# Optimization experiments

Measured on AMD Instinct MI355X. Metric: run time of the kernel, lower is better.

The kernel has to match this reference:

```python
import jax, jax.numpy as jnp
import numpy as np

N, E, B, H = 20000, 100000, 512, 64
IN_CH, EDGE_DIM, OUT_CH = 16, 8, 1


def setup_inputs() -> dict:
    key = jax.random.key(0)
    ks = jax.random.split(key, 20)
    rn = lambda k, shp, s=0.1: (jax.random.normal(k, shp, jnp.float32) * s)
    return {
        'x': rn(ks[0], (N, IN_CH), 1.0),
        'edge_index': jax.random.randint(ks[1], (2, E), 0, N),
        'edge_attr': rn(ks[2], (E, EDGE_DIM), 1.0),
        'batch': jnp.sort(jax.random.randint(ks[3], (N,), 0, B)),
        'lin0_w': rn(ks[4], (IN_CH, H)), 'lin0_b': jnp.zeros((H,), jnp.float32),
        'nn1_w': rn(ks[5], (EDGE_DIM, 128)), 'nn1_b': jnp.zeros((128,), jnp.float32),
        'nn2_w': rn(ks[6], (128, H * H), 0.02), 'nn2_b': jnp.zeros((H * H,), jnp.float32),
        'root_w': rn(ks[7], (H, H)), 'root_b': jnp.zeros((H,), jnp.float32),
        'gru_wih': rn(ks[8], (H, 3 * H)), 'gru_whh': rn(ks[9], (H, 3 * H)),
        'gru_bih': jnp.zeros((3 * H,), jnp.float32), 'gru_bhh': jnp.zeros((3 * H,), jnp.float32),
        'lstm_wih': rn(ks[10], (2 * H, 4 * H)), 'lstm_whh': rn(ks[11], (H, 4 * H)),
        'lstm_bih': jnp.zeros((4 * H,), jnp.float32), 'lstm_bhh': jnp.zeros((4 * H,), jnp.float32),
        'lin1_w': rn(ks[12], (2 * H, H)), 'lin1_b': jnp.zeros((H,), jnp.float32),
        'lin2_w': rn(ks[13], (H, OUT_CH)), 'lin2_b': jnp.zeros((OUT_CH,), jnp.float32),
    }


def reference(x, edge_index, edge_attr, batch, lin0_w, lin0_b, nn1_w, nn1_b,
              nn2_w, nn2_b, root_w, root_b, gru_wih, gru_whh, gru_bih, gru_bhh,
              lstm_wih, lstm_whh, lstm_bih, lstm_bhh, lin1_w, lin1_b, lin2_w, lin2_b):
    src, dst = edge_index[0], edge_index[1]
    # edge network weights (shared across the 3 message-passing steps)
    ew = jax.nn.relu(edge_attr @ nn1_w + nn1_b) @ nn2_w + nn2_b  # [E, H*H]
    ew = ew.reshape(E, H, H)
    deg = jnp.maximum(jax.ops.segment_sum(jnp.ones((E,), x.dtype), dst, N), 1.0)

    out = jax.nn.relu(x @ lin0_w + lin0_b)  # [N, H]
    h = out
    for _ in range(3):
        # NNConv: gather src feats, per-edge matvec, scatter-mean to dst, + root linear
        msg = jnp.einsum('ei,eio->eo', out[src], ew)                  # [E, H]
        agg = jax.ops.segment_sum(msg, dst, N) / deg[:, None]          # [N, H]
        m = jax.nn.relu(agg + out @ root_w + root_b)
        # GRU cell (torch gate order r, z, n)
        gi = m @ gru_wih + gru_bih
        gh = h @ gru_whh + gru_bhh
        r = jax.nn.sigmoid(gi[:, :H] + gh[:, :H])
        z = jax.nn.sigmoid(gi[:, H:2 * H] + gh[:, H:2 * H])
        n = jnp.tanh(gi[:, 2 * H:] + r * gh[:, 2 * H:])
        h = (1.0 - z) * n + z * h
        out = h

    # Set2Set pooling, 3 processing steps (torch LSTM gate order i, f, g, o)
    q_star = jnp.zeros((B, 2 * H), x.dtype)
    hh = jnp.zeros((B, H), x.dtype)
    cc = jnp.zeros((B, H), x.dtype)
    for _ in range(3):
        g = q_star @ lstm_wih + hh @ lstm_whh + lstm_bih + lstm_bhh    # [B, 4H]
        i_g = jax.nn.sigmoid(g[:, :H])
        f_g = jax.nn.sigmoid(g[:, H:2 * H])
        g_g = jnp.tanh(g[:, 2 * H:3 * H])
        o_g = jax.nn.sigmoid(g[:, 3 * H:])
        cc = f_g * cc + i_g * g_g
        hh = o_g * jnp.tanh(cc)
        q = hh                                                          # [B, H]
        e = jnp.sum(out * q[batch], axis=-1)                            # [N]
        e_max = jax.ops.segment_max(e, batch, B)
        a = jnp.exp(e - e_max[batch])
        a = a / jax.ops.segment_sum(a, batch, B)[batch]
        rvec = jax.ops.segment_sum(a[:, None] * out, batch, B)          # [B, H]
        q_star = jnp.concatenate([q, rvec], axis=-1)

    y = jax.nn.relu(q_star @ lin1_w + lin1_b) @ lin2_w + lin2_b         # [B, 1]
    return y
```

## Files before the change

kernel.cpp:

```cpp
#include <hip/hip_runtime.h>
#include <hip/hip_bf16.h>
#include <hip/hip_fp16.h>
#include <cstddef>
#include <cstdint>

#define N_NODES 20000
#define N_EDGES 100000
#define N_BATCH 512

#define EPB 96
#define TS 6
#define ECAP 100032

typedef __attribute__((ext_vector_type(8))) short ushort8_t;
typedef __attribute__((ext_vector_type(8))) _Float16 f16x8;
typedef __attribute__((ext_vector_type(4))) float f32x4;

union F16x8U { f16x8 v; unsigned int u[4]; };

__device__ __forceinline__ float sigmoidf_(float x) { return 1.f / (1.f + expf(-x)); }
__device__ __forceinline__ unsigned short f2h(float x) {
    return __half_as_ushort(__float2half(x));
}
__device__ __forceinline__ float h2f(unsigned short s) {
    return __half2float(__ushort_as_half(s));
}

#define LIN0_BLOCKS 5000
#define BSW_BLOCKS 258
#define CNT_BLOCKS 391

__global__ __launch_bounds__(256) void prep1_kernel(
        const float* __restrict__ x, const float* __restrict__ l0w, const float* __restrict__ l0b,
        const float* __restrict__ w2, const float* __restrict__ b2,
        const int* __restrict__ ei,
        float* __restrict__ out, unsigned short* __restrict__ bsw,
        int* __restrict__ cnt, int E) {
    int bid = blockIdx.x, tid = threadIdx.x;
    if (bid < LIN0_BLOCKS) {
        int idx = bid * 256 + tid;
        int n = idx >> 6, j = idx & 63;
        float acc = l0b[j];
#pragma unroll
        for (int i = 0; i < 16; i++) acc += x[n * 16 + i] * l0w[i * 64 + j];
        out[idx] = fmaxf(acc, 0.f);
    } else if (bid < LIN0_BLOCKS + BSW_BLOCKS) {
        int idx = (bid - LIN0_BLOCKS) * 256 + tid;
        if (idx < 66048) {
            int l = idx & 63, oc = (idx >> 6) & 3, ks = idx >> 8;
            int o = oc * 16 + (l & 15);
            int kap0 = ks * 32 + 8 * (l >> 4);
#pragma unroll
            for (int j = 0; j < 8; ++j) {
                int kap = kap0 + j;
                int k = kap >> 6, i = kap & 63;
                float v = (k < 128) ? w2[(size_t)k * 4096 + i * 64 + o] : b2[i * 64 + o];
                bsw[(size_t)idx * 8 + j] = f2h(v);
            }
        }
    } else {
        int e = (bid - LIN0_BLOCKS - BSW_BLOCKS) * 256 + tid;
        if (e < E) atomicAdd(&cnt[ei[E + e]], 1);
    }
}

__global__ __launch_bounds__(1024) void scan_kernel(const int* __restrict__ cnt,
                                                    int* __restrict__ cstart,
                                                    int* __restrict__ cursor,
                                                    float* __restrict__ degf, int n) {
    __shared__ int part[1024];
    int t = threadIdx.x;
    int base = t * 20;
    int loc[20];
    int s = 0;
#pragma unroll
    for (int i = 0; i < 20; ++i) {
        int idx = base + i;
        int c = (idx < n) ? cnt[idx] : 0;
        loc[i] = s;
        s += c;
    }
    part[t] = s;
    __syncthreads();
    for (int off = 1; off < 1024; off <<= 1) {
        int v = (t >= off) ? part[t - off] : 0;
        __syncthreads();
        part[t] += v;
        __syncthreads();
    }
    int tb = part[t] - s;
#pragma unroll
    for (int i = 0; i < 20; ++i) {
        int idx = base + i;
        if (idx < n) {
            int b0 = tb + loc[i];
            cstart[idx] = b0;
            cursor[idx] = b0;
            degf[idx] = (float)cnt[idx];
        }
    }
}

__global__ void place_kernel(const int* __restrict__ ei, const float* __restrict__ ea,
                             int* __restrict__ cursor,
                             int* __restrict__ src_s, float* __restrict__ ea_s, int E) {
    int e = blockIdx.x * 256 + threadIdx.x;
    if (e < E) {
        int dst = ei[E + e];
        int slot = atomicAdd(&cursor[dst], 1);
        src_s[slot] = ei[e];
        const float4* s = (const float4*)(ea + (size_t)e * 8);
        float4 a = s[0], b = s[1];
        float4* d = (float4*)(ea_s + (size_t)slot * 8);
        d[0] = a; d[1] = b;
    }
}

__global__ __launch_bounds__(256, 2) void msg_mfma(const float* __restrict__ out,
                                                   const float* __restrict__ ea_s,
                                                   const float* __restrict__ w1g,
                                                   const float* __restrict__ b1g,
                                                   const unsigned short* __restrict__ bsw,
                                                   const int* __restrict__ src_s,
                                                   unsigned short* __restrict__ msgp, int E) {
    __shared__ __align__(16) unsigned short hs16[128 * EPB];
    __shared__ __align__(16) float w1l[8 * 128];
    __shared__ __align__(16) float b1l[128];
    const int tid = threadIdx.x;
    const int w = tid >> 6, l = tid & 63;
    const int e0 = blockIdx.x * EPB;
    const int r16 = l & 15, q = l >> 4;

    {
        f32x4 v = *(const f32x4*)&w1g[tid * 4];
        *(f32x4*)&w1l[tid * 4] = v;
        if (tid < 32) *(f32x4*)&b1l[tid * 4] = *(const f32x4*)&b1g[tid * 4];
    }

    f16x8 sfrag[TS][2];
#pragma unroll
    for (int t = 0; t < TS; ++t) {
        int e = e0 + t * 16 + r16;
        int src = (e < E) ? src_s[e] : 0;
        const f32x4* p = (const f32x4*)(out + (size_t)src * 64);
#pragma unroll
        for (int st = 0; st < 2; ++st) {
            f16x8 f = {};
            if (e < E) {
                f32x4 a = p[st * 8 + q * 2], b = p[st * 8 + q * 2 + 1];
#pragma unroll
                for (int j = 0; j < 4; ++j) { f[j] = (_Float16)a[j]; f[4 + j] = (_Float16)b[j]; }
            }
            sfrag[t][st] = f;
        }
    }

    __syncthreads();

    if (tid < 192) {
        int ep = tid >> 1;
        int koff = (tid & 1) * 64;
        int e = e0 + ep;
        bool v = e < E;
        float ear[8];
        const float* earow = ea_s + (size_t)(v ? e : 0) * 8;
#pragma unroll
        for (int i = 0; i < 8; ++i) ear[i] = earow[i];
#pragma unroll
        for (int kv = 0; kv < 16; ++kv) {
            int k = koff + kv * 4;
            f32x4 a = *(const f32x4*)&b1l[k];
#pragma unroll
            for (int i = 0; i < 8; ++i) {
                f32x4 wv = *(const f32x4*)&w1l[i * 128 + k];
                a += ear[i] * wv;
            }
#pragma unroll
            for (int jj = 0; jj < 4; ++jj)
                hs16[(k + jj) * EPB + ep] = v ? f2h(fmaxf(a[jj], 0.f)) : (unsigned short)0;
        }
    }

    const f16x8* bp = (const f16x8*)bsw;
    f16x8 bfA[8], bfB[8];
#pragma unroll
    for (int i = 0; i < 8; ++i) bfA[i] = bp[((w * 8 + i) << 6) + l];

    __syncthreads();

    f32x4 acc[TS][4] = {};

#define MSG_COMPUTE(K, BF)                                                     \
    {                                                                          \
        _Pragma("unroll")                                                      \
        for (int t = 0; t < TS; ++t) {                                         \
            unsigned int hu = hs16[(K) * EPB + t * 16 + r16];                  \
            _Pragma("unroll")                                                  \
            for (int st = 0; st < 2; ++st) {                                   \
                F16x8U s_, a_;                                                 \
                s_.v = sfrag[t][st];                                           \
                asm("v_pk_mul_f16 %0, %1, %2 op_sel:[0,0] op_sel_hi:[0,1]"     \
                    : "=v"(a_.u[0]) : "v"(hu), "v"(s_.u[0]));                  \
                asm("v_pk_mul_f16 %0, %1, %2 op_sel:[0,0] op_sel_hi:[0,1]"     \
                    : "=v"(a_.u[1]) : "v"(hu), "v"(s_.u[1]));                  \
                asm("v_pk_mul_f16 %0, %1, %2 op_sel:[0,0] op_sel_hi:[0,1]"     \
                    : "=v"(a_.u[2]) : "v"(hu), "v"(s_.u[2]));                  \
                asm("v_pk_mul_f16 %0, %1, %2 op_sel:[0,0] op_sel_hi:[0,1]"     \
                    : "=v"(a_.u[3]) : "v"(hu), "v"(s_.u[3]));                  \
                _Pragma("unroll")                                              \
                for (int oc = 0; oc < 4; ++oc)                                 \
                    acc[t][oc] = __builtin_amdgcn_mfma_f32_16x16x32_f16(       \
                        a_.v, BF[st * 4 + oc], acc[t][oc], 0, 0, 0);           \
            }                                                                  \
        }                                                                      \
    }

#pragma unroll 1
    for (int kk = 0; kk < 16; ++kk) {
        int k1 = w + kk * 8;
        int k2 = k1 + 4;
#pragma unroll
        for (int i = 0; i < 8; ++i) bfB[i] = bp[((k2 * 8 + i) << 6) + l];
        MSG_COMPUTE(k1, bfA);
        if (kk < 15) {
            int k3 = k1 + 8;
#pragma unroll
            for (int i = 0; i < 8; ++i) bfA[i] = bp[((k3 * 8 + i) << 6) + l];
        }
        MSG_COMPUTE(k2, bfB);
    }
#undef MSG_COMPUTE

    if (w == 0) {
#pragma unroll
        for (int i = 0; i < 8; ++i) bfA[i] = bp[((128 * 8 + i) << 6) + l];
#pragma unroll
        for (int t = 0; t < TS; ++t)
#pragma unroll
            for (int st = 0; st < 2; ++st)
#pragma unroll
                for (int oc = 0; oc < 4; ++oc)
                    acc[t][oc] = __builtin_amdgcn_mfma_f32_16x16x32_f16(
                        sfrag[t][st], bfA[st * 4 + oc], acc[t][oc], 0, 0, 0);
    }

    unsigned short* slab = msgp + (size_t)w * ECAP * 64;
#pragma unroll
    for (int t = 0; t < TS; ++t) {
#pragma unroll
        for (int r = 0; r < 4; ++r) {
            int e = e0 + t * 16 + q * 4 + r;
            if (e < E) {
                unsigned short* row = slab + (size_t)e * 64 + r16;
                row[0]  = f2h(acc[t][0][r]);
                row[16] = f2h(acc[t][1][r]);
                row[32] = f2h(acc[t][2][r]);
                row[48] = f2h(acc[t][3][r]);
            }
        }
    }
}

__global__ __launch_bounds__(256) void gru_kernel(float* __restrict__ out,
                                                  const unsigned short* __restrict__ msgp,
                                                  const int* __restrict__ cstart,
                                                  const int* __restrict__ cnt,
                                                  const float* __restrict__ deg,
                                                  const float* __restrict__ root_w,
                                                  const float* __restrict__ root_b,
                                                  const float* __restrict__ wih,
                                                  const float* __restrict__ whh,
                                                  const float* __restrict__ bih,
                                                  const float* __restrict__ bhh) {
    int w = threadIdx.x >> 6, j = threadIdx.x & 63;
    int n = blockIdx.x * 4 + w;
    __shared__ float s_o[4][64];
    __shared__ float s_m[4][64];
    s_o[w][j] = out[(size_t)n * 64 + j];
    __syncthreads();

    float msum = 0.f;
    {
        int base = cstart[n], c = cnt[n];
        for (int s2 = 0; s2 < c; ++s2) {
            size_t slot = (size_t)(base + s2) * 64 + j;
            float a0 = h2f(msgp[slot]);
            float a1 = h2f(msgp[(size_t)ECAP * 64 + slot]);
            float a2 = h2f(msgp[2 * (size_t)ECAP * 64 + slot]);
            float a3 = h2f(msgp[3 * (size_t)ECAP * 64 + slot]);
            msum += (a0 + a1) + (a2 + a3);
        }
    }
    float d = deg[n]; if (d < 1.f) d = 1.f;
    float mv = msum / d + root_b[j];
#pragma unroll 8
    for (int i = 0; i < 64; i++) mv += s_o[w][i] * root_w[i * 64 + j];
    mv = fmaxf(mv, 0.f);
    s_m[w][j] = mv;
    __syncthreads();
    float gi_r = bih[j], gi_z = bih[64 + j], gi_n = bih[128 + j];
    float gh_r = bhh[j], gh_z = bhh[64 + j], gh_n = bhh[128 + j];
#pragma unroll 4
    for (int i = 0; i < 64; i++) {
        float m = s_m[w][i], hv = s_o[w][i];
        gi_r += m * wih[i * 192 + j];
        gi_z += m * wih[i * 192 + 64 + j];
        gi_n += m * wih[i * 192 + 128 + j];
        gh_r += hv * whh[i * 192 + j];
        gh_z += hv * whh[i * 192 + 64 + j];
        gh_n += hv * whh[i * 192 + 128 + j];
    }
    float r = sigmoidf_(gi_r + gh_r);
    float z = sigmoidf_(gi_z + gh_z);
    float nn = tanhf(gi_n + r * gh_n);
    float hnew = (1.f - z) * nn + z * s_o[w][j];
    out[(size_t)n * 64 + j] = hnew;
}

__global__ __launch_bounds__(256) void s2s_final(const float* __restrict__ out,
                                                 const int* __restrict__ batch,
                                                 const float* __restrict__ wih,
                                                 const float* __restrict__ whh,
                                                 const float* __restrict__ bih,
                                                 const float* __restrict__ bhh,
                                                 const float* __restrict__ w1,
                                                 const float* __restrict__ b1,
                                                 const float* __restrict__ w2,
                                                 const float* __restrict__ b2,
                                                 float* __restrict__ y, int N) {
    int b = blockIdx.x;
    int tid = threadIdx.x;
    int gate = tid >> 6, j = tid & 63;
    __shared__ float s_qs[128];
    __shared__ float s_g[4][64];
    __shared__ float s_h[64];
    __shared__ float s_c[64];
    __shared__ int s_lo, s_hi;
    __shared__ float s_red[4];
    __shared__ float s_rv[4][64];

    if (tid < 128) s_qs[tid] = 0.f;
    if (gate == 2) s_h[j] = 0.f;
    if (gate == 3) s_c[j] = 0.f;
    if (tid == 0) {
        int lo = 0, hi = N;
        while (lo < hi) { int mid = (lo + hi) >> 1; if (batch[mid] < b) lo = mid + 1; else hi = mid; }
        s_lo = lo;
        int lo2 = lo, hi2 = N;
        while (lo2 < hi2) { int mid = (lo2 + hi2) >> 1; if (batch[mid] < b + 1) lo2 = mid + 1; else hi2 = mid; }
        s_hi = lo2;
    }
    __syncthreads();

    for (int it = 0; it < 3; ++it) {
        float g = bih[gate * 64 + j] + bhh[gate * 64 + j];
#pragma unroll 4
        for (int i = 0; i < 128; ++i) g += s_qs[i] * wih[i * 256 + gate * 64 + j];
#pragma unroll 4
        for (int i = 0; i < 64; ++i) g += s_h[i] * whh[i * 256 + gate * 64 + j];
        s_g[gate][j] = g;
        __syncthreads();
        if (gate == 0) {
            float c = sigmoidf_(s_g[1][j]) * s_c[j] + sigmoidf_(s_g[0][j]) * tanhf(s_g[2][j]);
            float h = sigmoidf_(s_g[3][j]) * tanhf(c);
            s_c[j] = c;
            s_h[j] = h;
            s_qs[j] = h;
        }
        __syncthreads();

        int lo = s_lo, hi = s_hi;
        float wmax = -3.402823e38f;
        for (int n = lo + gate; n < hi; n += 4) {
            float p = out[(size_t)n * 64 + j] * s_h[j];
#pragma unroll
            for (int d = 32; d >= 1; d >>= 1) p += __shfl_xor(p, d);
            wmax = fmaxf(wmax, p);
        }
        if (j == 0) s_red[gate] = wmax;
        __syncthreads();
        float m = fmaxf(fmaxf(s_red[0], s_red[1]), fmaxf(s_red[2], s_red[3]));
        __syncthreads();
        float ssum = 0.f, rv = 0.f;
        for (int n = lo + gate; n < hi; n += 4) {
            float xv = out[(size_t)n * 64 + j];
            float p = xv * s_h[j];
#pragma unroll
            for (int d = 32; d >= 1; d >>= 1) p += __shfl_xor(p, d);
            float a = expf(p - m);
            ssum += a;
            rv += a * xv;
        }
        if (j == 0) s_red[gate] = ssum;
        s_rv[gate][j] = rv;
        __syncthreads();
        if (gate == 0) {
            float S = s_red[0] + s_red[1] + s_red[2] + s_red[3];
            float r = s_rv[0][j] + s_rv[1][j] + s_rv[2][j] + s_rv[3][j];
            s_qs[64 + j] = (S > 0.f) ? r / S : 0.f;
        }
        __syncthreads();
    }

    if (gate == 0) {
        float tv = b1[j];
#pragma unroll 4
        for (int i = 0; i < 128; ++i) tv += s_qs[i] * w1[i * 64 + j];
        tv = fmaxf(tv, 0.f);
        float p = tv * w2[j];
#pragma unroll
        for (int d = 32; d >= 1; d >>= 1) p += __shfl_xor(p, d);
        if (j == 0) y[b] = p + b2[0];
    }
}

extern "C" void kernel_launch(void* const* d_in, const int* in_sizes, int n_in,
                              void* d_out, int out_size, void* d_ws, size_t ws_size,
                              hipStream_t stream) {
    const int N = N_NODES, E = N_EDGES, B = N_BATCH;
    const float* x       = (const float*)d_in[0];
    const int*   ei      = (const int*)d_in[1];
    const float* ea      = (const float*)d_in[2];
    const int*   batch   = (const int*)d_in[3];
    const float* lin0_w  = (const float*)d_in[4];
    const float* lin0_b  = (const float*)d_in[5];
    const float* nn1_w   = (const float*)d_in[6];
    const float* nn1_b   = (const float*)d_in[7];
    const float* nn2_w   = (const float*)d_in[8];
    const float* nn2_b   = (const float*)d_in[9];
    const float* root_w  = (const float*)d_in[10];
    const float* root_b  = (const float*)d_in[11];
    const float* gru_wih = (const float*)d_in[12];
    const float* gru_whh = (const float*)d_in[13];
    const float* gru_bih = (const float*)d_in[14];
    const float* gru_bhh = (const float*)d_in[15];
    const float* lstm_wih = (const float*)d_in[16];
    const float* lstm_whh = (const float*)d_in[17];
    const float* lstm_bih = (const float*)d_in[18];
    const float* lstm_bhh = (const float*)d_in[19];
    const float* lin1_w  = (const float*)d_in[20];
    const float* lin1_b  = (const float*)d_in[21];
    const float* lin2_w  = (const float*)d_in[22];
    const float* lin2_b  = (const float*)d_in[23];
    float* y = (float*)d_out;

    char* ws = (char*)d_ws;
    size_t off = 0;
    auto alloc = [&](size_t bytes) { void* p = ws + off; off = (off + bytes + 255) & ~(size_t)255; return p; };
    unsigned short* bsw  = (unsigned short*)alloc((size_t)66048 * 8 * 2);
    unsigned short* msgp = (unsigned short*)alloc((size_t)4 * ECAP * 64 * 2);
    float* ea_s   = (float*)alloc((size_t)ECAP * 8 * 4);
    float* out    = (float*)alloc((size_t)N * 64 * 4);
    float* deg    = (float*)alloc((size_t)N * 4);
    int*   cnt    = (int*)alloc((size_t)N * 4);
    int*   cstart = (int*)alloc((size_t)N * 4);
    int*   cursor = (int*)alloc((size_t)N * 4);
    int*   src_s  = (int*)alloc((size_t)E * 4);

    hipMemsetAsync(cnt, 0, (size_t)N * 4, stream);

    prep1_kernel<<<LIN0_BLOCKS + BSW_BLOCKS + CNT_BLOCKS, 256, 0, stream>>>(
        x, lin0_w, lin0_b, nn2_w, nn2_b, ei, out, bsw, cnt, E);
    scan_kernel<<<1, 1024, 0, stream>>>(cnt, cstart, cursor, deg, N);
    place_kernel<<<(E + 255) / 256, 256, 0, stream>>>(ei, ea, cursor, src_s, ea_s, E);

    for (int step = 0; step < 3; ++step) {
        msg_mfma<<<(E + EPB - 1) / EPB, 256, 0, stream>>>(out, ea_s, nn1_w, nn1_b,
                                                          bsw, src_s, msgp, E);
        gru_kernel<<<N / 4, 256, 0, stream>>>(out, msgp, cstart, cnt, deg, root_w, root_b,
                                              gru_wih, gru_whh, gru_bih, gru_bhh);
    }

    s2s_final<<<B, 256, 0, stream>>>(out, batch, lstm_wih, lstm_whh, lstm_bih, lstm_bhh,
                                     lin1_w, lin1_b, lin2_w, lin2_b, y, N);
}
```

Measured before the change: 671.7 us.

## Split msg_mfma by edges across waves with LDS double-buffered weight staging

Before, each wave handled a slice of the hidden dimension k for all 96 edges in the block, and wrote a partial-sum slab that the GRU kernel had to add up across four slabs. Now each wave owns 32 of the 128 edges in the block and loops over all 129 k values. The nn2 weight fragments are staged into LDS with global_load_lds, double-buffered and separated by barriers. The root/bias term is folded in by adding a constant-one row to hs16, and a single message buffer removes the four-slab write and read traffic. The cost is a block barrier on every k iteration and fewer MFMA tiles per wave, with occupancy raised to 3 blocks per multiprocessor to hide the latency.

```diff
diff --git a/kernel.cpp b/kernel.cpp
--- a/kernel.cpp
+++ b/kernel.cpp
@@ -8,9 +8,8 @@
 #define N_EDGES 100000
 #define N_BATCH 512
 
-#define EPB 96
-#define TS 6
-#define ECAP 100032
+#define EPB 128
+#define ECAP 100096
 
 typedef __attribute__((ext_vector_type(8))) short ushort8_t;
 typedef __attribute__((ext_vector_type(8))) _Float16 f16x8;
@@ -116,20 +115,23 @@
     }
 }
 
-__global__ __launch_bounds__(256, 2) void msg_mfma(const float* __restrict__ out,
+__global__ __launch_bounds__(256, 3) void msg_mfma(const float* __restrict__ out,
                                                    const float* __restrict__ ea_s,
                                                    const float* __restrict__ w1g,
                                                    const float* __restrict__ b1g,
                                                    const unsigned short* __restrict__ bsw,
                                                    const int* __restrict__ src_s,
                                                    unsigned short* __restrict__ msgp, int E) {
-    __shared__ __align__(16) unsigned short hs16[128 * EPB];
-    __shared__ __align__(16) float w1l[8 * 128];
-    __shared__ __align__(16) float b1l[128];
+    __shared__ __align__(16) unsigned short hs16[129 * EPB];
+    __shared__ __align__(16) unsigned char bbuf[2 * 8192];
+    float* w1l = (float*)bbuf;
+    float* b1l = (float*)(bbuf + 4096);
+
     const int tid = threadIdx.x;
     const int w = tid >> 6, l = tid & 63;
     const int e0 = blockIdx.x * EPB;
     const int r16 = l & 15, q = l >> 4;
+    const int w32 = w * 32;
 
     {
         f32x4 v = *(const f32x4*)&w1g[tid * 4];
@@ -137,10 +139,10 @@
         if (tid < 32) *(f32x4*)&b1l[tid * 4] = *(const f32x4*)&b1g[tid * 4];
     }
 
-    f16x8 sfrag[TS][2];
-#pragma unroll
-    for (int t = 0; t < TS; ++t) {
-        int e = e0 + t * 16 + r16;
+    f16x8 sfrag[2][2];
+#pragma unroll
+    for (int t = 0; t < 2; ++t) {
+        int e = e0 + w32 + t * 16 + r16;
         int src = (e < E) ? src_s[e] : 0;
         const f32x4* p = (const f32x4*)(out + (size_t)src * 64);
 #pragma unroll
@@ -157,9 +159,9 @@
 
     __syncthreads();
 
-    if (tid < 192) {
-        int ep = tid >> 1;
-        int koff = (tid & 1) * 64;
+    {
+        int ep = tid & 127;
+        int koff = (tid >> 7) * 64;
         int e = e0 + ep;
         bool v = e < E;
         float ear[8];
@@ -179,22 +181,36 @@
             for (int jj = 0; jj < 4; ++jj)
                 hs16[(k + jj) * EPB + ep] = v ? f2h(fmaxf(a[jj], 0.f)) : (unsigned short)0;
         }
-    }
-
-    const f16x8* bp = (const f16x8*)bsw;
-    f16x8 bfA[8], bfB[8];
-#pragma unroll
-    for (int i = 0; i < 8; ++i) bfA[i] = bp[((w * 8 + i) << 6) + l];
-
-    __syncthreads();
-
-    f32x4 acc[TS][4] = {};
-
-#define MSG_COMPUTE(K, BF)                                                     \
+        if (koff == 0)
+            hs16[128 * EPB + ep] = v ? (unsigned short)0x3C00 : (unsigned short)0;
+    }
+
+    __syncthreads();
+
+    typedef __attribute__((address_space(3))) void lds_t;
+    typedef const __attribute__((address_space(1))) void gm_t;
+
+#define STAGE(SLOT, BUF)                                                       \
     {                                                                          \
         _Pragma("unroll")                                                      \
-        for (int t = 0; t < TS; ++t) {                                         \
-            unsigned int hu = hs16[(K) * EPB + t * 16 + r16];                  \
+        for (int i = 0; i < 2; ++i) {                                          \
+            int fr = 2 * w + i;                                                \
+            const unsigned short* g = bsw + (((size_t)(SLOT) * 8 + fr) * 64 + l) * 8; \
+            __builtin_amdgcn_global_load_lds((gm_t*)g,                         \
+                (lds_t*)(bbuf + (BUF) * 8192 + fr * 1024), 16, 0, 0);          \
+        }                                                                      \
+    }
+
+#define COMPUTE(K, BUF)                                                        \
+    {                                                                          \
+        const f16x8* bP = (const f16x8*)(bbuf + (BUF) * 8192);                 \
+        f16x8 bf[8];                                                           \
+        _Pragma("unroll")                                                      \
+        for (int i = 0; i < 8; ++i) bf[i] = bP[i * 64 + l];                    \
+        __builtin_amdgcn_s_setprio(1);                                         \
+        _Pragma("unroll")                                                      \
+        for (int t = 0; t < 2; ++t) {                                          \
+            unsigned int hu = hs16[(K) * EPB + w32 + t * 16 + r16];            \
             _Pragma("unroll")                                                  \
             for (int st = 0; st < 2; ++st) {                                   \
                 F16x8U s_, a_;                                                 \
@@ -210,48 +226,40 @@
                 _Pragma("unroll")                                              \
                 for (int oc = 0; oc < 4; ++oc)                                 \
                     acc[t][oc] = __builtin_amdgcn_mfma_f32_16x16x32_f16(       \
-                        a_.v, BF[st * 4 + oc], acc[t][oc], 0, 0, 0);           \
+                        a_.v, bf[st * 4 + oc], acc[t][oc], 0, 0, 0);           \
             }                                                                  \
         }                                                                      \
-    }
+        __builtin_amdgcn_s_setprio(0);                                         \
+    }
+
+    STAGE(0, 0);
+
+    f32x4 acc[2][4] = {};
 
 #pragma unroll 1
-    for (int kk = 0; kk < 16; ++kk) {
-        int k1 = w + kk * 8;
-        int k2 = k1 + 4;
-#pragma unroll
-        for (int i = 0; i < 8; ++i) bfB[i] = bp[((k2 * 8 + i) << 6) + l];
-        MSG_COMPUTE(k1, bfA);
-        if (kk < 15) {
-            int k3 = k1 + 8;
-#pragma unroll
-            for (int i = 0; i < 8; ++i) bfA[i] = bp[((k3 * 8 + i) << 6) + l];
-        }
-        MSG_COMPUTE(k2, bfB);
-    }
-#undef MSG_COMPUTE
-
-    if (w == 0) {
-#pragma unroll
-        for (int i = 0; i < 8; ++i) bfA[i] = bp[((128 * 8 + i) << 6) + l];
-#pragma unroll
-        for (int t = 0; t < TS; ++t)
-#pragma unroll
-            for (int st = 0; st < 2; ++st)
-#pragma unroll
-                for (int oc = 0; oc < 4; ++oc)
-                    acc[t][oc] = __builtin_amdgcn_mfma_f32_16x16x32_f16(
-                        sfrag[t][st], bfA[st * 4 + oc], acc[t][oc], 0, 0, 0);
-    }
-
-    unsigned short* slab = msgp + (size_t)w * ECAP * 64;
-#pragma unroll
-    for (int t = 0; t < TS; ++t) {
+    for (int k = 0; k < 128; ++k) {
+        STAGE(k + 1, (k + 1) & 1);
+        asm volatile("s_waitcnt vmcnt(2)" ::: "memory");
+        __builtin_amdgcn_s_barrier();
+        __builtin_amdgcn_sched_barrier(0);
+        COMPUTE(k, k & 1);
+        __builtin_amdgcn_s_barrier();
+    }
+    asm volatile("s_waitcnt vmcnt(0)" ::: "memory");
+    __builtin_amdgcn_s_barrier();
+    __builtin_amdgcn_sched_barrier(0);
+    COMPUTE(128, 0);
+
+#undef STAGE
+#undef COMPUTE
+
+#pragma unroll
+    for (int t = 0; t < 2; ++t) {
 #pragma unroll
         for (int r = 0; r < 4; ++r) {
-            int e = e0 + t * 16 + q * 4 + r;
+            int e = e0 + w32 + t * 16 + q * 4 + r;
             if (e < E) {
-                unsigned short* row = slab + (size_t)e * 64 + r16;
+                unsigned short* row = msgp + (size_t)e * 64 + r16;
                 row[0]  = f2h(acc[t][0][r]);
                 row[16] = f2h(acc[t][1][r]);
                 row[32] = f2h(acc[t][2][r]);
@@ -282,14 +290,8 @@
     float msum = 0.f;
     {
         int base = cstart[n], c = cnt[n];
-        for (int s2 = 0; s2 < c; ++s2) {
-            size_t slot = (size_t)(base + s2) * 64 + j;
-            float a0 = h2f(msgp[slot]);
-            float a1 = h2f(msgp[(size_t)ECAP * 64 + slot]);
-            float a2 = h2f(msgp[2 * (size_t)ECAP * 64 + slot]);
-            float a3 = h2f(msgp[3 * (size_t)ECAP * 64 + slot]);
-            msum += (a0 + a1) + (a2 + a3);
-        }
+        for (int s2 = 0; s2 < c; ++s2)
+            msum += h2f(msgp[(size_t)(base + s2) * 64 + j]);
     }
     float d = deg[n]; if (d < 1.f) d = 1.f;
     float mv = msum / d + root_b[j];
@@ -448,7 +450,7 @@
     size_t off = 0;
     auto alloc = [&](size_t bytes) { void* p = ws + off; off = (off + bytes + 255) & ~(size_t)255; return p; };
     unsigned short* bsw  = (unsigned short*)alloc((size_t)66048 * 8 * 2);
-    unsigned short* msgp = (unsigned short*)alloc((size_t)4 * ECAP * 64 * 2);
+    unsigned short* msgp = (unsigned short*)alloc((size_t)ECAP * 64 * 2);
     float* ea_s   = (float*)alloc((size_t)ECAP * 8 * 4);
     float* out    = (float*)alloc((size_t)N * 64 * 4);
     float* deg    = (float*)alloc((size_t)N * 4);
```

Measured after the change: 776.2 us. 1.16x slower.
